# Optimization experiments

Measured on AMD Instinct MI355X. Metric: run time of the kernel, lower is better.

Reference implementation:

```python
import jax, jax.numpy as jnp
import numpy as np

BATCH, IN_DIM, OUT_DIM = 8192, 4096, 4096
BASE_LR = 0.015
PRED_ERR = 0.0


def setup_inputs() -> dict:
    key = jax.random.key(0)
    ks = jax.random.split(key, 6)
    x = jax.random.normal(ks[0], (BATCH, IN_DIM), jnp.float32)
    # W_slow ~ orthogonal init with gain 1.4 (approximated by scaled gaussian)
    W_slow = jax.random.normal(ks[1], (OUT_DIM, IN_DIM), jnp.float32) * (1.4 / np.sqrt(IN_DIM))
    W_fast = jax.random.normal(ks[2], (OUT_DIM, IN_DIM), jnp.float32) * 0.01
    gamma = jnp.ones((OUT_DIM,), jnp.float32)
    beta = jnp.zeros((OUT_DIM,), jnp.float32)
    w1 = jax.random.normal(ks[3], (16, 2), jnp.float32) * 0.5
    b1 = jnp.zeros((16,), jnp.float32)
    w2 = jax.random.normal(ks[4], (1, 16), jnp.float32) * 0.5
    b2 = jnp.full((1,), -2.0, jnp.float32)  # plasticity_controller[2].bias = -2.0
    global_plasticity = jnp.float32(0.5)
    return {"x": x, "W_slow": W_slow, "W_fast": W_fast, "gamma": gamma,
            "beta": beta, "w1": w1, "b1": b1, "w2": w2, "b2": b2,
            "global_plasticity": global_plasticity}


def reference(x, W_slow, W_fast, gamma, beta, w1, b1, w2, b2, global_plasticity):
    # dual linear sum: slow + fast pathway, [B, out_dim]
    pre_act = x @ W_slow.T + x @ W_fast.T

    # per-output-column batch stats (torch std is unbiased, ddof=1)
    batch_mean = pre_act.mean(axis=0)                       # [out_dim]
    batch_std = pre_act.std(axis=0, ddof=1) + 1e-6          # [out_dim]
    stats = jnp.stack([batch_mean, batch_std], axis=1)      # [out_dim, 2]

    # tiny 2-16-1 plasticity controller MLP
    h = jnp.tanh(stats @ w1.T + b1)                          # [out_dim, 16]
    learned_plasticity = jax.nn.sigmoid(h @ w2.T + b2)[:, 0] # [out_dim]
    eff = global_plasticity * learned_plasticity * (1.0 - PRED_ERR)

    # LayerNorm (eps=1e-5) + soft-clipped tanh output
    mu = pre_act.mean(axis=-1, keepdims=True)
    var = pre_act.var(axis=-1, keepdims=True)
    ln = (pre_act - mu) * jax.lax.rsqrt(var + 1e-5) * gamma + beta
    out = 5.0 * jnp.tanh(ln / 5.0)

    # Hebbian fast-weight update (training branch), functional version
    B = x.shape[0]
    x_norm = (x ** 2).sum(axis=1).mean() + 1e-6
    correlation = (out.T @ x) / B                            # [out_dim, in_dim]
    forgetting = 0.2 * W_fast
    delta = jnp.clip(correlation / x_norm - forgetting, -0.05, 0.05)
    lr_vector = eff[:, None] * BASE_LR
    W_fast_updated = (W_fast + delta * lr_vector) * 0.999
    new_W_fast = jnp.where(eff.mean() > 0.001, W_fast_updated, W_fast)

    return out, new_W_fast
```

## Files before the change

kernel.cpp:

```cpp
#include <hip/hip_runtime.h>
#include <stdint.h>

#define B_DIM 8192
#define K_DIM 4096
#define N_DIM 4096

typedef unsigned short u16;
typedef float f4 __attribute__((ext_vector_type(4)));
typedef float f32x4 __attribute__((ext_vector_type(4)));
typedef __bf16 bf16x8 __attribute__((ext_vector_type(8)));
typedef unsigned short u16x8 __attribute__((ext_vector_type(8)));
typedef unsigned short u16x4 __attribute__((ext_vector_type(4)));

#define AS1(p) ((const __attribute__((address_space(1))) void*)(p))
#define AS3(p) ((__attribute__((address_space(3))) void*)(p))

__device__ __forceinline__ u16 f2bf(float f) {
  uint32_t u = __builtin_bit_cast(uint32_t, f);
  u += 0x7fffu + ((u >> 16) & 1u);
  return (u16)(u >> 16);
}

__device__ __forceinline__ float wred(float v) {
#pragma unroll
  for (int o = 32; o > 0; o >>= 1) v += __shfl_xor(v, o);
  return v;
}

__global__ void k_init(float* __restrict__ stats) {
  for (int i = threadIdx.x; i < 8194; i += 256) stats[i] = 0.0f;
}

__global__ __launch_bounds__(256) void k_prep_w(const f4* __restrict__ wslow, const f4* __restrict__ wfast,
                                                u16x4* __restrict__ wo) {
  size_t stride = (size_t)gridDim.x * 256;
  size_t n4 = (size_t)N_DIM * K_DIM / 4;
  for (size_t i = (size_t)blockIdx.x * 256 + threadIdx.x; i < n4; i += stride) {
    f4 a = wslow[i], b = wfast[i];
    u16x4 o;
#pragma unroll
    for (int j = 0; j < 4; ++j) o[j] = f2bf(a[j] + b[j]);
    wo[i] = o;
  }
}

__global__ __launch_bounds__(256) void k_prep_x(const f4* __restrict__ x, u16x4* __restrict__ xb,
                                                float* __restrict__ xsumsq) {
  __shared__ float red[4];
  size_t stride = (size_t)gridDim.x * 256;
  size_t n4 = (size_t)B_DIM * K_DIM / 4;
  float s = 0.f;
  for (size_t i = (size_t)blockIdx.x * 256 + threadIdx.x; i < n4; i += stride) {
    f4 v = x[i];
    u16x4 o;
#pragma unroll
    for (int j = 0; j < 4; ++j) { o[j] = f2bf(v[j]); s += v[j] * v[j]; }
    xb[i] = o;
  }
  s = wred(s);
  int lane = threadIdx.x & 63, wave = threadIdx.x >> 6;
  if (lane == 0) red[wave] = s;
  __syncthreads();
  if (threadIdx.x == 0) atomicAdd(xsumsq, red[0] + red[1] + red[2] + red[3]);
}

__global__ __launch_bounds__(512, 2) void gemm8(const u16* __restrict__ A, const u16* __restrict__ Bm,
                                                float* __restrict__ C, int M, int N, int K) {
  __shared__ __align__(16) u16 As[32768];
  __shared__ __align__(16) u16 Bs[32768];

  const int tid = threadIdx.x, wave = tid >> 6, lane = tid & 63;
  const int li = lane & 15, hi = lane >> 4;
  const int wm = wave >> 2, wn = wave & 3;

  const int GX = N >> 8;
  const int nwg = GX * (M >> 8);
  int bid = blockIdx.y * GX + blockIdx.x;
  int swz = (bid & 7) * (nwg >> 3) + (bid >> 3);
  const int bx = swz % GX, by = swz / GX;
  const int m0 = by * 256, n0 = bx * 256;

  int srcoff[2][2];
#pragma unroll
  for (int h = 0; h < 2; ++h)
#pragma unroll
    for (int q = 0; q < 2; ++q) {
      int O = h * 16384 + q * 8192 + wave * 1024 + lane * 16;
      int T = O ^ (((O >> 7) & 7) << 4);
      srcoff[h][q] = (T >> 7) * K + ((T & 127) >> 1);
    }

  const u16* Abase = A + (size_t)m0 * K;
  const u16* Bbase = Bm + (size_t)n0 * K;

#define STG_A(buf, h, kt) do { \
  __builtin_amdgcn_global_load_lds(AS1(Abase + (kt) + srcoff[h][0]), AS3(&As[(buf)*16384 + (h)*8192 + wave*512]), 16, 0, 0); \
  __builtin_amdgcn_global_load_lds(AS1(Abase + (kt) + srcoff[h][1]), AS3(&As[(buf)*16384 + (h)*8192 + 4096 + wave*512]), 16, 0, 0); \
} while (0)
#define STG_B(buf, h, kt) do { \
  __builtin_amdgcn_global_load_lds(AS1(Bbase + (kt) + srcoff[h][0]), AS3(&Bs[(buf)*16384 + (h)*8192 + wave*512]), 16, 0, 0); \
  __builtin_amdgcn_global_load_lds(AS1(Bbase + (kt) + srcoff[h][1]), AS3(&Bs[(buf)*16384 + (h)*8192 + 4096 + wave*512]), 16, 0, 0); \
} while (0)

  const int xa = (li & 7) << 3;
  const int abase = (wm * 128 + li) * 64 + hi * 8;
  const int bbase = (wn * 64 + li) * 64 + hi * 8;
#define LDA_(dst, buf, m, ks) dst = *(const bf16x8*)&As[(buf)*16384 + (((abase + (m)*1024 + (ks)*32)) ^ xa)]
#define LDB_(dst, buf, n, ks) dst = *(const bf16x8*)&Bs[(buf)*16384 + (((bbase + (n)*1024 + (ks)*32)) ^ xa)]

  f32x4 acc[8][4] = {};
  bf16x8 a[8][2], b[4][2];
  const int NT = K >> 6;

  STG_A(0, 0, 0); STG_A(0, 1, 0); STG_B(0, 0, 0); STG_B(0, 1, 0);
  STG_A(1, 0, 64); STG_A(1, 1, 64); STG_B(1, 0, 64);
  asm volatile("s_waitcnt vmcnt(6)" ::: "memory");
  __builtin_amdgcn_s_barrier();

  for (int t = 0; t < NT; ++t) {
    const int buf = t & 1;
    const int ktn = (t + 1) << 6, ktnn = (t + 2) << 6;

#pragma unroll
    for (int m = 0; m < 4; ++m) { LDA_(a[m][0], buf, m, 0); LDA_(a[m][1], buf, m, 1); }
#pragma unroll
    for (int n = 0; n < 2; ++n) { LDB_(b[n][0], buf, n, 0); LDB_(b[n][1], buf, n, 1); }
    if (t + 1 < NT) STG_B(buf ^ 1, 1, ktn);
    __builtin_amdgcn_s_barrier();
    asm volatile("s_waitcnt lgkmcnt(0)" ::: "memory");
    __builtin_amdgcn_sched_barrier(0);
    __builtin_amdgcn_s_setprio(1);
#pragma unroll
    for (int ks = 0; ks < 2; ++ks)
#pragma unroll
      for (int m = 0; m < 4; ++m)
#pragma unroll
        for (int n = 0; n < 2; ++n)
          acc[m][n] = __builtin_amdgcn_mfma_f32_16x16x32_bf16(a[m][ks], b[n][ks], acc[m][n], 0, 0, 0);
    __builtin_amdgcn_s_setprio(0);
    __builtin_amdgcn_s_barrier();

#pragma unroll
    for (int m = 4; m < 8; ++m) { LDA_(a[m][0], buf, m, 0); LDA_(a[m][1], buf, m, 1); }
    __builtin_amdgcn_s_barrier();
    asm volatile("s_waitcnt lgkmcnt(0)" ::: "memory");
    __builtin_amdgcn_sched_barrier(0);
    __builtin_amdgcn_s_setprio(1);
#pragma unroll
    for (int ks = 0; ks < 2; ++ks)
#pragma unroll
      for (int m = 4; m < 8; ++m)
#pragma unroll
        for (int n = 0; n < 2; ++n)
          acc[m][n] = __builtin_amdgcn_mfma_f32_16x16x32_bf16(a[m][ks], b[n][ks], acc[m][n], 0, 0, 0);
    __builtin_amdgcn_s_setprio(0);
    __builtin_amdgcn_s_barrier();

#pragma unroll
    for (int n = 2; n < 4; ++n) { LDB_(b[n][0], buf, n, 0); LDB_(b[n][1], buf, n, 1); }
    if (t + 2 < NT) { STG_A(buf, 0, ktnn); STG_A(buf, 1, ktnn); }
    __builtin_amdgcn_s_barrier();
    asm volatile("s_waitcnt lgkmcnt(0)" ::: "memory");
    __builtin_amdgcn_sched_barrier(0);
    __builtin_amdgcn_s_setprio(1);
#pragma unroll
    for (int ks = 0; ks < 2; ++ks)
#pragma unroll
      for (int m = 0; m < 4; ++m)
#pragma unroll
        for (int n = 2; n < 4; ++n)
          acc[m][n] = __builtin_amdgcn_mfma_f32_16x16x32_bf16(a[m][ks], b[n][ks], acc[m][n], 0, 0, 0);
    __builtin_amdgcn_s_setprio(0);
    __builtin_amdgcn_s_barrier();

    if (t + 2 < NT) STG_B(buf, 0, ktnn);
    __builtin_amdgcn_s_barrier();
    __builtin_amdgcn_s_setprio(1);
#pragma unroll
    for (int ks = 0; ks < 2; ++ks)
#pragma unroll
      for (int m = 4; m < 8; ++m)
#pragma unroll
        for (int n = 2; n < 4; ++n)
          acc[m][n] = __builtin_amdgcn_mfma_f32_16x16x32_bf16(a[m][ks], b[n][ks], acc[m][n], 0, 0, 0);
    __builtin_amdgcn_s_setprio(0);
    if (t + 1 < NT) {
      if (t + 2 < NT) asm volatile("s_waitcnt vmcnt(6)" ::: "memory");
      else            asm volatile("s_waitcnt vmcnt(0)" ::: "memory");
    }
    __builtin_amdgcn_s_barrier();
  }

  float* Cp = C + (size_t)(m0 + wm * 128 + hi * 4) * N + n0 + wn * 64 + li;
#pragma unroll
  for (int m = 0; m < 8; ++m)
#pragma unroll
    for (int n = 0; n < 4; ++n)
#pragma unroll
      for (int j = 0; j < 4; ++j)
        Cp[(size_t)(m * 16 + j) * N + n * 16] = acc[m][n][j];
#undef STG_A
#undef STG_B
#undef LDA_
#undef LDB_
}

__global__ __launch_bounds__(256) void k_colstats(const float* __restrict__ pre,
                                                  float* __restrict__ colsum, float* __restrict__ colsumsq) {
  int col = blockIdx.x * 256 + threadIdx.x;
  int r0 = blockIdx.y * 128;
  const float* p = pre + (size_t)r0 * N_DIM + col;
  float s = 0.f, q = 0.f;
#pragma unroll 4
  for (int i = 0; i < 128; ++i) {
    float v = p[(size_t)i * N_DIM];
    s += v; q += v * v;
  }
  atomicAdd(&colsum[col], s);
  atomicAdd(&colsumsq[col], q);
}

__global__ __launch_bounds__(256) void k_mlp(const float* __restrict__ colsum, const float* __restrict__ colsumsq,
                                             const float* __restrict__ w1, const float* __restrict__ b1,
                                             const float* __restrict__ w2, const float* __restrict__ b2,
                                             const float* __restrict__ gp, float* __restrict__ eff,
                                             float* __restrict__ effsum) {
  __shared__ float red[4];
  int c = blockIdx.x * 256 + threadIdx.x;
  float mean = colsum[c] * (1.0f / B_DIM);
  float var = (colsumsq[c] - (float)B_DIM * mean * mean) * (1.0f / (B_DIM - 1));
  float sd = sqrtf(fmaxf(var, 0.f)) + 1e-6f;
  float acc = b2[0];
#pragma unroll
  for (int i = 0; i < 16; ++i) {
    float h = tanhf(mean * w1[2 * i] + sd * w1[2 * i + 1] + b1[i]);
    acc += h * w2[i];
  }
  float p = 1.0f / (1.0f + expf(-acc));
  float e = gp[0] * p;
  eff[c] = e;
  float s = wred(e);
  int lane = threadIdx.x & 63, wave = threadIdx.x >> 6;
  if (lane == 0) red[wave] = s;
  __syncthreads();
  if (threadIdx.x == 0) atomicAdd(effsum, red[0] + red[1] + red[2] + red[3]);
}

__global__ __launch_bounds__(256) void k_ln(const float* __restrict__ pre, const float* __restrict__ gamma,
                                            const float* __restrict__ beta, float* __restrict__ outF,
                                            u16* __restrict__ outB) {
  __shared__ float row[N_DIM];
  __shared__ float red[2][4];
  int t = threadIdx.x, lane = t & 63, wave = t >> 6;
  const float* p = pre + (size_t)blockIdx.x * N_DIM;
  float s = 0.f;
#pragma unroll
  for (int q = 0; q < 4; ++q) {
    int c = (q * 256 + t) * 4;
    f4 v = *(const f4*)&p[c];
    *(f4*)&row[c] = v;
    s += v[0] + v[1] + v[2] + v[3];
  }
  s = wred(s);
  if (lane == 0) red[0][wave] = s;
  __syncthreads();
  float mean = (red[0][0] + red[0][1] + red[0][2] + red[0][3]) * (1.0f / N_DIM);
  float vs = 0.f;
#pragma unroll
  for (int q = 0; q < 4; ++q) {
    int c = (q * 256 + t) * 4;
    f4 v = *(const f4*)&row[c];
#pragma unroll
    for (int j = 0; j < 4; ++j) { float d = v[j] - mean; vs += d * d; }
  }
  vs = wred(vs);
  if (lane == 0) red[1][wave] = vs;
  __syncthreads();
  float var = (red[1][0] + red[1][1] + red[1][2] + red[1][3]) * (1.0f / N_DIM);
  float rstd = rsqrtf(var + 1e-5f);
  float* o = outF + (size_t)blockIdx.x * N_DIM;
  u16* ob = outB + (size_t)blockIdx.x * N_DIM;
#pragma unroll
  for (int q = 0; q < 4; ++q) {
    int c = (q * 256 + t) * 4;
    f4 v = *(const f4*)&row[c];
    f4 g = *(const f4*)&gamma[c];
    f4 be = *(const f4*)&beta[c];
    f4 r;
    u16x4 rb;
#pragma unroll
    for (int j = 0; j < 4; ++j) {
      float ln = (v[j] - mean) * rstd * g[j] + be[j];
      float ov = 5.0f * tanhf(ln * 0.2f);
      r[j] = ov; rb[j] = f2bf(ov);
    }
    *(f4*)&o[c] = r;
    *(u16x4*)&ob[c] = rb;
  }
}

__global__ __launch_bounds__(256) void k_transpose(const u16* __restrict__ src, u16* __restrict__ dst,
                                                   int R, int C) {
  __shared__ u16 tile[64][65];
  int tc = blockIdx.x, tr = blockIdx.y;
  int t = threadIdx.x;
#pragma unroll
  for (int q = 0; q < 2; ++q) {
    int idx = q * 256 + t;
    int row = idx >> 3, cg = idx & 7;
    u16x8 v = *(const u16x8*)&src[(size_t)(tr * 64 + row) * C + tc * 64 + cg * 8];
#pragma unroll
    for (int j = 0; j < 8; ++j) tile[row][cg * 8 + j] = v[j];
  }
  __syncthreads();
#pragma unroll
  for (int q = 0; q < 2; ++q) {
    int idx = q * 256 + t;
    int row = idx >> 3, cg = idx & 7;
    u16x8 v;
#pragma unroll
    for (int j = 0; j < 8; ++j) v[j] = tile[cg * 8 + j][row];
    *(u16x8*)&dst[(size_t)(tc * 64 + row) * R + tr * 64 + cg * 8] = v;
  }
}

__global__ __launch_bounds__(256) void k_update(const float* __restrict__ corr, const float* __restrict__ wf,
                                                const float* __restrict__ eff, const float* __restrict__ sc,
                                                float* __restrict__ out_wf) {
  float xn = sc[0] * (1.0f / B_DIM) + 1e-6f;
  float inv = 1.0f / ((float)B_DIM * xn);
  bool on = (sc[1] * (1.0f / N_DIM)) > 0.001f;
  size_t i = ((size_t)blockIdx.x * 256 + threadIdx.x) * 4;
  int n = (int)(i >> 12);
  float lr = eff[n] * 0.015f;
  f4 c4 = *(const f4*)&corr[i];
  f4 w4 = *(const f4*)&wf[i];
  f4 r;
#pragma unroll
  for (int j = 0; j < 4; ++j) {
    float delta = fminf(fmaxf(c4[j] * inv - 0.2f * w4[j], -0.05f), 0.05f);
    r[j] = on ? (w4[j] + delta * lr) * 0.999f : w4[j];
  }
  *(f4*)&out_wf[i] = r;
}

extern "C" void kernel_launch(void* const* d_in, const int* in_sizes, int n_in,
                              void* d_out, int out_size, void* d_ws, size_t ws_size,
                              hipStream_t stream) {
  const float* x      = (const float*)d_in[0];
  const float* W_slow = (const float*)d_in[1];
  const float* W_fast = (const float*)d_in[2];
  const float* gamma  = (const float*)d_in[3];
  const float* beta   = (const float*)d_in[4];
  const float* w1     = (const float*)d_in[5];
  const float* b1     = (const float*)d_in[6];
  const float* w2     = (const float*)d_in[7];
  const float* b2     = (const float*)d_in[8];
  const float* gp     = (const float*)d_in[9];

  float* outF = (float*)d_out;
  float* outW = (float*)d_out + (size_t)B_DIM * N_DIM;

  uint8_t* ws = (uint8_t*)d_ws;
  u16*  x_bf   = (u16*)(ws + 0);
  u16*  outT   = (u16*)(ws + 0);
  u16*  wsum   = (u16*)(ws + 67108864);
  u16*  out_bf = (u16*)(ws + 67108864);
  u16*  xT     = (u16*)(ws + 134217728);
  float* stats = (float*)(ws + 201326592);
  float* colsum   = stats;
  float* colsumsq = stats + 4096;
  float* xsumsq   = stats + 8192;
  float* effsum   = stats + 8193;
  float* eff      = stats + 8448;

  k_init<<<1, 256, 0, stream>>>(stats);
  k_prep_w<<<2048, 256, 0, stream>>>((const f4*)W_slow, (const f4*)W_fast, (u16x4*)wsum);
  k_prep_x<<<2048, 256, 0, stream>>>((const f4*)x, (u16x4*)x_bf, xsumsq);
  gemm8<<<dim3(N_DIM / 256, B_DIM / 256), 512, 0, stream>>>(x_bf, wsum, outF, B_DIM, N_DIM, K_DIM);
  k_colstats<<<dim3(N_DIM / 256, B_DIM / 128), 256, 0, stream>>>(outF, colsum, colsumsq);
  k_mlp<<<N_DIM / 256, 256, 0, stream>>>(colsum, colsumsq, w1, b1, w2, b2, gp, eff, effsum);
  k_ln<<<B_DIM, 256, 0, stream>>>(outF, gamma, beta, outF, out_bf);
  k_transpose<<<dim3(K_DIM / 64, B_DIM / 64), 256, 0, stream>>>(x_bf, xT, B_DIM, K_DIM);
  k_transpose<<<dim3(N_DIM / 64, B_DIM / 64), 256, 0, stream>>>(out_bf, outT, B_DIM, N_DIM);
  gemm8<<<dim3(K_DIM / 256, N_DIM / 256), 512, 0, stream>>>(outT, xT, outW, N_DIM, K_DIM, B_DIM);
  k_update<<<(N_DIM * K_DIM / 4) / 256, 256, 0, stream>>>(outW, W_fast, eff, xsumsq, outW);
}
```

Baseline: 739.8 us.

## Restructure GEMM main loop into ping-pong register-buffered schedule with fewer barriers

```diff
diff --git a/kernel.cpp b/kernel.cpp
--- a/kernel.cpp
+++ b/kernel.cpp
@@ -109,86 +109,83 @@
 #define LDB_(dst, buf, n, ks) dst = *(const bf16x8*)&Bs[(buf)*16384 + (((bbase + (n)*1024 + (ks)*32)) ^ xa)]
 
   f32x4 acc[8][4] = {};
-  bf16x8 a[8][2], b[4][2];
+  bf16x8 a0[4][2], a1[4][2], b0[2][2], b1[2][2];
   const int NT = K >> 6;
 
   STG_A(0, 0, 0); STG_A(0, 1, 0); STG_B(0, 0, 0); STG_B(0, 1, 0);
-  STG_A(1, 0, 64); STG_A(1, 1, 64); STG_B(1, 0, 64);
-  asm volatile("s_waitcnt vmcnt(6)" ::: "memory");
+  STG_A(1, 0, 64); STG_A(1, 1, 64); STG_B(1, 0, 64); STG_B(1, 1, 64);
+  asm volatile("s_waitcnt vmcnt(8)" ::: "memory");
   __builtin_amdgcn_s_barrier();
-
-  for (int t = 0; t < NT; ++t) {
-    const int buf = t & 1;
-    const int ktn = (t + 1) << 6, ktnn = (t + 2) << 6;
-
-#pragma unroll
-    for (int m = 0; m < 4; ++m) { LDA_(a[m][0], buf, m, 0); LDA_(a[m][1], buf, m, 1); }
-#pragma unroll
-    for (int n = 0; n < 2; ++n) { LDB_(b[n][0], buf, n, 0); LDB_(b[n][1], buf, n, 1); }
-    if (t + 1 < NT) STG_B(buf ^ 1, 1, ktn);
-    __builtin_amdgcn_s_barrier();
-    asm volatile("s_waitcnt lgkmcnt(0)" ::: "memory");
-    __builtin_amdgcn_sched_barrier(0);
-    __builtin_amdgcn_s_setprio(1);
-#pragma unroll
-    for (int ks = 0; ks < 2; ++ks)
-#pragma unroll
-      for (int m = 0; m < 4; ++m)
-#pragma unroll
-        for (int n = 0; n < 2; ++n)
-          acc[m][n] = __builtin_amdgcn_mfma_f32_16x16x32_bf16(a[m][ks], b[n][ks], acc[m][n], 0, 0, 0);
-    __builtin_amdgcn_s_setprio(0);
-    __builtin_amdgcn_s_barrier();
-
-#pragma unroll
-    for (int m = 4; m < 8; ++m) { LDA_(a[m][0], buf, m, 0); LDA_(a[m][1], buf, m, 1); }
-    __builtin_amdgcn_s_barrier();
-    asm volatile("s_waitcnt lgkmcnt(0)" ::: "memory");
-    __builtin_amdgcn_sched_barrier(0);
-    __builtin_amdgcn_s_setprio(1);
-#pragma unroll
-    for (int ks = 0; ks < 2; ++ks)
-#pragma unroll
-      for (int m = 4; m < 8; ++m)
-#pragma unroll
-        for (int n = 0; n < 2; ++n)
-          acc[m][n] = __builtin_amdgcn_mfma_f32_16x16x32_bf16(a[m][ks], b[n][ks], acc[m][n], 0, 0, 0);
-    __builtin_amdgcn_s_setprio(0);
-    __builtin_amdgcn_s_barrier();
-
-#pragma unroll
-    for (int n = 2; n < 4; ++n) { LDB_(b[n][0], buf, n, 0); LDB_(b[n][1], buf, n, 1); }
-    if (t + 2 < NT) { STG_A(buf, 0, ktnn); STG_A(buf, 1, ktnn); }
-    __builtin_amdgcn_s_barrier();
-    asm volatile("s_waitcnt lgkmcnt(0)" ::: "memory");
-    __builtin_amdgcn_sched_barrier(0);
-    __builtin_amdgcn_s_setprio(1);
-#pragma unroll
-    for (int ks = 0; ks < 2; ++ks)
-#pragma unroll
-      for (int m = 0; m < 4; ++m)
-#pragma unroll
-        for (int n = 2; n < 4; ++n)
-          acc[m][n] = __builtin_amdgcn_mfma_f32_16x16x32_bf16(a[m][ks], b[n][ks], acc[m][n], 0, 0, 0);
-    __builtin_amdgcn_s_setprio(0);
-    __builtin_amdgcn_s_barrier();
-
-    if (t + 2 < NT) STG_B(buf, 0, ktnn);
-    __builtin_amdgcn_s_barrier();
-    __builtin_amdgcn_s_setprio(1);
-#pragma unroll
-    for (int ks = 0; ks < 2; ++ks)
-#pragma unroll
-      for (int m = 4; m < 8; ++m)
-#pragma unroll
-        for (int n = 2; n < 4; ++n)
-          acc[m][n] = __builtin_amdgcn_mfma_f32_16x16x32_bf16(a[m][ks], b[n][ks], acc[m][n], 0, 0, 0);
-    __builtin_amdgcn_s_setprio(0);
-    if (t + 1 < NT) {
-      if (t + 2 < NT) asm volatile("s_waitcnt vmcnt(6)" ::: "memory");
-      else            asm volatile("s_waitcnt vmcnt(0)" ::: "memory");
-    }
-    __builtin_amdgcn_s_barrier();
+#pragma unroll
+  for (int m = 0; m < 4; ++m) { LDA_(a0[m][0], 0, m, 0); LDA_(a0[m][1], 0, m, 1); }
+
+#define TILE_BODY(B_, t_) do {                                                      \
+    const int kt2 = ((t_) + 2) << 6;                                                \
+                                \
+    LDB_(b0[0][0], B_, 0, 0); LDB_(b0[0][1], B_, 0, 1);                             \
+    LDB_(b0[1][0], B_, 1, 0); LDB_(b0[1][1], B_, 1, 1);                             \
+    LDB_(b1[0][0], B_, 2, 0); LDB_(b1[0][1], B_, 2, 1);                             \
+    LDB_(b1[1][0], B_, 3, 0); LDB_(b1[1][1], B_, 3, 1);                             \
+    __builtin_amdgcn_sched_barrier(0);                                              \
+    __builtin_amdgcn_s_setprio(1);                                                  \
+    _Pragma("unroll")                                                               \
+    for (int ks = 0; ks < 2; ++ks)                                                  \
+      _Pragma("unroll")                                                             \
+      for (int m = 0; m < 4; ++m)                                                   \
+        _Pragma("unroll")                                                           \
+        for (int n = 0; n < 2; ++n)                                                 \
+          acc[m][n] = __builtin_amdgcn_mfma_f32_16x16x32_bf16(a0[m][ks], b0[n][ks], acc[m][n], 0, 0, 0); \
+    __builtin_amdgcn_s_setprio(0);                                                  \
+    __builtin_amdgcn_s_barrier();                                                   \
+                                   \
+    _Pragma("unroll")                                                               \
+    for (int m = 0; m < 4; ++m) { LDA_(a1[m][0], B_, m + 4, 0); LDA_(a1[m][1], B_, m + 4, 1); } \
+    __builtin_amdgcn_sched_barrier(0);                                              \
+    __builtin_amdgcn_s_setprio(1);                                                  \
+    _Pragma("unroll")                                                               \
+    for (int ks = 0; ks < 2; ++ks)                                                  \
+      _Pragma("unroll")                                                             \
+      for (int m = 0; m < 4; ++m)                                                   \
+        _Pragma("unroll")                                                           \
+        for (int n = 2; n < 4; ++n)                                                 \
+          acc[m][n] = __builtin_amdgcn_mfma_f32_16x16x32_bf16(a0[m][ks], b1[n - 2][ks], acc[m][n], 0, 0, 0); \
+    __builtin_amdgcn_s_setprio(0);                                                  \
+    __builtin_amdgcn_s_barrier();                                                   \
+     \
+    if ((t_) + 2 < NT) { STG_B(B_, 0, kt2); STG_B(B_, 1, kt2); }                    \
+    __builtin_amdgcn_sched_barrier(0);                                              \
+    __builtin_amdgcn_s_setprio(1);                                                  \
+    _Pragma("unroll")                                                               \
+    for (int ks = 0; ks < 2; ++ks)                                                  \
+      _Pragma("unroll")                                                             \
+      for (int m = 4; m < 8; ++m)                                                   \
+        _Pragma("unroll")                                                           \
+        for (int n = 2; n < 4; ++n)                                                 \
+          acc[m][n] = __builtin_amdgcn_mfma_f32_16x16x32_bf16(a1[m - 4][ks], b1[n - 2][ks], acc[m][n], 0, 0, 0); \
+    __builtin_amdgcn_s_setprio(0);                                                  \
+    if ((t_) + 2 < NT) asm volatile("s_waitcnt vmcnt(4)" ::: "memory");             \
+    else               asm volatile("s_waitcnt vmcnt(0)" ::: "memory");             \
+    __builtin_amdgcn_s_barrier();                                                   \
+     \
+    _Pragma("unroll")                                                               \
+    for (int m = 0; m < 4; ++m) { LDA_(a0[m][0], (B_) ^ 1, m, 0); LDA_(a0[m][1], (B_) ^ 1, m, 1); } \
+    if ((t_) + 2 < NT) { STG_A(B_, 0, kt2); STG_A(B_, 1, kt2); }                    \
+    __builtin_amdgcn_sched_barrier(0);                                              \
+    __builtin_amdgcn_s_setprio(1);                                                  \
+    _Pragma("unroll")                                                               \
+    for (int ks = 0; ks < 2; ++ks)                                                  \
+      _Pragma("unroll")                                                             \
+      for (int m = 4; m < 8; ++m)                                                   \
+        _Pragma("unroll")                                                           \
+        for (int n = 0; n < 2; ++n)                                                 \
+          acc[m][n] = __builtin_amdgcn_mfma_f32_16x16x32_bf16(a1[m - 4][ks], b0[n][ks], acc[m][n], 0, 0, 0); \
+    __builtin_amdgcn_s_setprio(0);                                                  \
+    __builtin_amdgcn_s_barrier();                                                   \
+  } while (0)
+
+  for (int t = 0; t < NT; t += 2) {
+    TILE_BODY(0, t);
+    TILE_BODY(1, t + 1);
   }
 
   float* Cp = C + (size_t)(m0 + wm * 128 + hi * 4) * N + n0 + wn * 64 + li;
@@ -199,6 +196,7 @@
 #pragma unroll
       for (int j = 0; j < 4; ++j)
         Cp[(size_t)(m * 16 + j) * N + n * 16] = acc[m][n][j];
+#undef TILE_BODY
 #undef STG_A
 #undef STG_B
 #undef LDA_
```

After: 1.442 ms. 95.0% more time.

## Fuse column stats and Hebbian update into GEMM epilogues, merge x transpose

Applied to the files above, without the earlier changes.

```diff
diff --git a/kernel.cpp b/kernel.cpp
--- a/kernel.cpp
+++ b/kernel.cpp
@@ -44,28 +44,44 @@
   }
 }
 
-__global__ __launch_bounds__(256) void k_prep_x(const f4* __restrict__ x, u16x4* __restrict__ xb,
-                                                float* __restrict__ xsumsq) {
+__global__ __launch_bounds__(256) void k_prep_xT(const float* __restrict__ x, u16* __restrict__ xb,
+                                                 u16* __restrict__ xT, float* __restrict__ xsumsq) {
+  __shared__ u16 tile[64][68];
   __shared__ float red[4];
-  size_t stride = (size_t)gridDim.x * 256;
-  size_t n4 = (size_t)B_DIM * K_DIM / 4;
+  int tk = blockIdx.x, tb = blockIdx.y;
+  int t = threadIdx.x;
   float s = 0.f;
-  for (size_t i = (size_t)blockIdx.x * 256 + threadIdx.x; i < n4; i += stride) {
-    f4 v = x[i];
+#pragma unroll
+  for (int q = 0; q < 4; ++q) {
+    int idx = q * 256 + t;
+    int row = idx >> 4, cg = idx & 15;
+    f4 v = *(const f4*)&x[(size_t)(tb * 64 + row) * K_DIM + tk * 64 + cg * 4];
     u16x4 o;
 #pragma unroll
     for (int j = 0; j < 4; ++j) { o[j] = f2bf(v[j]); s += v[j] * v[j]; }
-    xb[i] = o;
+    *(u16x4*)&xb[(size_t)(tb * 64 + row) * K_DIM + tk * 64 + cg * 4] = o;
+    *(u16x4*)&tile[row][cg * 4] = o;
   }
   s = wred(s);
-  int lane = threadIdx.x & 63, wave = threadIdx.x >> 6;
-  if (lane == 0) red[wave] = s;
+  if ((t & 63) == 0) red[t >> 6] = s;
   __syncthreads();
-  if (threadIdx.x == 0) atomicAdd(xsumsq, red[0] + red[1] + red[2] + red[3]);
+  if (t == 0) atomicAdd(xsumsq, red[0] + red[1] + red[2] + red[3]);
+#pragma unroll
+  for (int q = 0; q < 2; ++q) {
+    int idx = q * 256 + t;
+    int row = idx >> 3, cg = idx & 7;
+    u16x8 v;
+#pragma unroll
+    for (int j = 0; j < 8; ++j) v[j] = tile[cg * 8 + j][row];
+    *(u16x8*)&xT[(size_t)(tk * 64 + row) * B_DIM + tb * 64 + cg * 8] = v;
+  }
 }
 
 __global__ __launch_bounds__(512, 2) void gemm8(const u16* __restrict__ A, const u16* __restrict__ Bm,
-                                                float* __restrict__ C, int M, int N, int K) {
+                                                float* __restrict__ C, int M, int N, int K,
+                                                float* __restrict__ colsum, float* __restrict__ colsumsq,
+                                                const float* __restrict__ wfast, const float* __restrict__ eff,
+                                                const float* __restrict__ sc) {
   __shared__ __align__(16) u16 As[32768];
   __shared__ __align__(16) u16 Bs[32768];
 
@@ -191,33 +207,58 @@
     __builtin_amdgcn_s_barrier();
   }
 
-  float* Cp = C + (size_t)(m0 + wm * 128 + hi * 4) * N + n0 + wn * 64 + li;
-#pragma unroll
-  for (int m = 0; m < 8; ++m)
-#pragma unroll
-    for (int n = 0; n < 4; ++n)
-#pragma unroll
-      for (int j = 0; j < 4; ++j)
-        Cp[(size_t)(m * 16 + j) * N + n * 16] = acc[m][n][j];
+  if (wfast) {
+    float xn = sc[0] * (1.0f / 8192.0f) + 1e-6f;
+    float inv = 1.0f / (8192.0f * xn);
+    bool on = (sc[1] * (1.0f / 4096.0f)) > 0.001f;
+    const int colb = n0 + wn * 64 + li;
+    const int rowb = m0 + wm * 128 + hi * 4;
+#pragma unroll
+    for (int m = 0; m < 8; ++m) {
+      f4 e4 = *(const f4*)&eff[rowb + m * 16];
+#pragma unroll
+      for (int j = 0; j < 4; ++j) {
+        float lr = e4[j] * 0.015f;
+        const size_t ro = (size_t)(rowb + m * 16 + j) * N;
+#pragma unroll
+        for (int n = 0; n < 4; ++n) {
+          float w = wfast[ro + colb + n * 16];
+          float delta = fminf(fmaxf(acc[m][n][j] * inv - 0.2f * w, -0.05f), 0.05f);
+          C[ro + colb + n * 16] = on ? (w + delta * lr) * 0.999f : w;
+        }
+      }
+    }
+  } else {
+    float* Cp = C + (size_t)(m0 + wm * 128 + hi * 4) * N + n0 + wn * 64 + li;
+#pragma unroll
+    for (int m = 0; m < 8; ++m)
+#pragma unroll
+      for (int n = 0; n < 4; ++n)
+#pragma unroll
+        for (int j = 0; j < 4; ++j)
+          Cp[(size_t)(m * 16 + j) * N + n * 16] = acc[m][n][j];
+    if (colsum) {
+#pragma unroll
+      for (int n = 0; n < 4; ++n) {
+        float s = 0.f, q = 0.f;
+#pragma unroll
+        for (int m = 0; m < 8; ++m)
+#pragma unroll
+          for (int j = 0; j < 4; ++j) { float v = acc[m][n][j]; s += v; q += v * v; }
+        s += __shfl_xor(s, 16); s += __shfl_xor(s, 32);
+        q += __shfl_xor(q, 16); q += __shfl_xor(q, 32);
+        if (hi == 0) {
+          int col = n0 + wn * 64 + n * 16 + li;
+          atomicAdd(&colsum[col], s);
+          atomicAdd(&colsumsq[col], q);
+        }
+      }
+    }
+  }
 #undef STG_A
 #undef STG_B
 #undef LDA_
 #undef LDB_
-}
-
-__global__ __launch_bounds__(256) void k_colstats(const float* __restrict__ pre,
-                                                  float* __restrict__ colsum, float* __restrict__ colsumsq) {
-  int col = blockIdx.x * 256 + threadIdx.x;
-  int r0 = blockIdx.y * 128;
-  const float* p = pre + (size_t)r0 * N_DIM + col;
-  float s = 0.f, q = 0.f;
-#pragma unroll 4
-  for (int i = 0; i < 128; ++i) {
-    float v = p[(size_t)i * N_DIM];
-    s += v; q += v * v;
-  }
-  atomicAdd(&colsum[col], s);
-  atomicAdd(&colsumsq[col], q);
 }
 
 __global__ __launch_bounds__(256) void k_mlp(const float* __restrict__ colsum, const float* __restrict__ colsumsq,
@@ -322,26 +363,6 @@
     for (int j = 0; j < 8; ++j) v[j] = tile[cg * 8 + j][row];
     *(u16x8*)&dst[(size_t)(tc * 64 + row) * R + tr * 64 + cg * 8] = v;
   }
-}
-
-__global__ __launch_bounds__(256) void k_update(const float* __restrict__ corr, const float* __restrict__ wf,
-                                                const float* __restrict__ eff, const float* __restrict__ sc,
-                                                float* __restrict__ out_wf) {
-  float xn = sc[0] * (1.0f / B_DIM) + 1e-6f;
-  float inv = 1.0f / ((float)B_DIM * xn);
-  bool on = (sc[1] * (1.0f / N_DIM)) > 0.001f;
-  size_t i = ((size_t)blockIdx.x * 256 + threadIdx.x) * 4;
-  int n = (int)(i >> 12);
-  float lr = eff[n] * 0.015f;
-  f4 c4 = *(const f4*)&corr[i];
-  f4 w4 = *(const f4*)&wf[i];
-  f4 r;
-#pragma unroll
-  for (int j = 0; j < 4; ++j) {
-    float delta = fminf(fmaxf(c4[j] * inv - 0.2f * w4[j], -0.05f), 0.05f);
-    r[j] = on ? (w4[j] + delta * lr) * 0.999f : w4[j];
-  }
-  *(f4*)&out_wf[i] = r;
 }
 
 extern "C" void kernel_launch(void* const* d_in, const int* in_sizes, int n_in,
@@ -376,13 +397,12 @@
 
   k_init<<<1, 256, 0, stream>>>(stats);
   k_prep_w<<<2048, 256, 0, stream>>>((const f4*)W_slow, (const f4*)W_fast, (u16x4*)wsum);
-  k_prep_x<<<2048, 256, 0, stream>>>((const f4*)x, (u16x4*)x_bf, xsumsq);
-  gemm8<<<dim3(N_DIM / 256, B_DIM / 256), 512, 0, stream>>>(x_bf, wsum, outF, B_DIM, N_DIM, K_DIM);
-  k_colstats<<<dim3(N_DIM / 256, B_DIM / 128), 256, 0, stream>>>(outF, colsum, colsumsq);
+  k_prep_xT<<<dim3(K_DIM / 64, B_DIM / 64), 256, 0, stream>>>(x, x_bf, xT, xsumsq);
+  gemm8<<<dim3(N_DIM / 256, B_DIM / 256), 512, 0, stream>>>(x_bf, wsum, outF, B_DIM, N_DIM, K_DIM,
+                                                            colsum, colsumsq, nullptr, nullptr, nullptr);
   k_mlp<<<N_DIM / 256, 256, 0, stream>>>(colsum, colsumsq, w1, b1, w2, b2, gp, eff, effsum);
   k_ln<<<B_DIM, 256, 0, stream>>>(outF, gamma, beta, outF, out_bf);
-  k_transpose<<<dim3(K_DIM / 64, B_DIM / 64), 256, 0, stream>>>(x_bf, xT, B_DIM, K_DIM);
   k_transpose<<<dim3(N_DIM / 64, B_DIM / 64), 256, 0, stream>>>(out_bf, outT, B_DIM, N_DIM);
-  gemm8<<<dim3(K_DIM / 256, N_DIM / 256), 512, 0, stream>>>(outT, xT, outW, N_DIM, K_DIM, B_DIM);
-  k_update<<<(N_DIM * K_DIM / 4) / 256, 256, 0, stream>>>(outW, W_fast, eff, xsumsq, outW);
-}
+  gemm8<<<dim3(K_DIM / 256, N_DIM / 256), 512, 0, stream>>>(outT, xT, outW, N_DIM, K_DIM, B_DIM,
+                                                            nullptr, nullptr, W_fast, eff, xsumsq);
+}
```

Measured after the change: 758.3 us. 1.03x slower.
